# Kernel tuning notes

Hardware: AMD Instinct MI355X
Metric: run time of the kernel (lower is better)

Reference implementation:

```python
import jax, jax.numpy as jnp
import numpy as np

EMBED_DIM = 1024
NUM_HEADS = 16
HEAD_DIM = EMBED_DIM // NUM_HEADS
WINDOW = 128


def setup_inputs() -> dict:
    key = jax.random.key(0)
    ks = jax.random.split(key, 11)
    B, S, E = 2, 2048, EMBED_DIM
    scale = 1.0 / np.sqrt(E)
    inp = {
        "q": jax.random.normal(ks[0], (B, S, E), jnp.float32),
        "k": jax.random.normal(ks[1], (B, S, E), jnp.float32),
        "v": jax.random.normal(ks[2], (B, S, E), jnp.float32),
        "Wq": jax.random.normal(ks[3], (E, E), jnp.float32) * scale,
        "bq": jnp.zeros((E,), jnp.float32),
        "Wk": jax.random.normal(ks[4], (E, E), jnp.float32) * scale,
        "bk": jnp.zeros((E,), jnp.float32),
        "Wv": jax.random.normal(ks[5], (E, E), jnp.float32) * scale,
        "bv": jnp.zeros((E,), jnp.float32),
        "Wo": jax.random.normal(ks[6], (E, E), jnp.float32) * scale,
        "bo": jnp.zeros((E,), jnp.float32),
    }
    return inp


def reference(q, k, v, Wq, bq, Wk, bk, Wv, bv, Wo, bo):
    B, S, E = q.shape
    H, D = NUM_HEADS, HEAD_DIM
    # projections (torch Linear: x @ W.T + b)
    Q = (q @ Wq.T + bq).reshape(B, S, H, D).transpose(0, 2, 1, 3)  # [B,H,S,D]
    K = (k @ Wk.T + bk).reshape(B, S, H, D).transpose(0, 2, 1, 3)
    V = (v @ Wv.T + bv).reshape(B, S, H, D).transpose(0, 2, 1, 3)
    scores = jnp.einsum("bhqd,bhkd->bhqk", Q, K) / jnp.sqrt(jnp.float32(D))
    idx = jnp.arange(S)
    band = jnp.abs(idx[:, None] - idx[None, :]) <= WINDOW  # [S,S] bool band mask
    scores = jnp.where(band[None, None], scores, -jnp.inf)
    probs = jax.nn.softmax(scores, axis=-1)
    out = jnp.einsum("bhqk,bhkd->bhqd", probs, V)  # [B,H,S,D]
    out = out.transpose(0, 2, 1, 3).reshape(B, S, E)
    return out @ Wo.T + bo
```

## Files before the change

kernel.cpp:

```cpp
#include <hip/hip_runtime.h>


#define S_LEN 2048
#define EMB   1024
#define NHEAD 16
#define HDIM  64
#define MROWS 4096

typedef __attribute__((ext_vector_type(4))) float f32x4;
typedef __attribute__((ext_vector_type(8))) short bf16x8;

__device__ __forceinline__ unsigned short f2bf(float x){
  union { float f; unsigned u; } un; un.f = x;
  unsigned u = un.u;
  unsigned r = (u + 0x7FFFu + ((u >> 16) & 1u)) >> 16;
  return (unsigned short)r;
}

__global__ __launch_bounds__(256) void cvt3_kernel(
    const float4* __restrict__ s0, const float4* __restrict__ s1,
    const float4* __restrict__ s2,
    unsigned long long* __restrict__ d0, unsigned long long* __restrict__ d1,
    unsigned long long* __restrict__ d2)
{
  int i = blockIdx.x * 256 + threadIdx.x;
  const float4* s = (blockIdx.y == 0) ? s0 : (blockIdx.y == 1) ? s1 : s2;
  unsigned long long* d = (blockIdx.y == 0) ? d0 : (blockIdx.y == 1) ? d1 : d2;
  float4 v = s[i];
  d[i] = (unsigned long long)f2bf(v.x)
       | ((unsigned long long)f2bf(v.y) << 16)
       | ((unsigned long long)f2bf(v.z) << 32)
       | ((unsigned long long)f2bf(v.w) << 48);
}

__global__ __launch_bounds__(256) void cvt4_kernel(
    const float4* __restrict__ s0, const float4* __restrict__ s1,
    const float4* __restrict__ s2, const float4* __restrict__ s3,
    unsigned long long* __restrict__ d0, unsigned long long* __restrict__ d1,
    unsigned long long* __restrict__ d2, unsigned long long* __restrict__ d3)
{
  int i = blockIdx.x * 256 + threadIdx.x;
  const float4* s = (blockIdx.y == 0) ? s0 : (blockIdx.y == 1) ? s1 :
                    (blockIdx.y == 2) ? s2 : s3;
  unsigned long long* d = (blockIdx.y == 0) ? d0 : (blockIdx.y == 1) ? d1 :
                          (blockIdx.y == 2) ? d2 : d3;
  float4 v = s[i];
  d[i] = (unsigned long long)f2bf(v.x)
       | ((unsigned long long)f2bf(v.y) << 16)
       | ((unsigned long long)f2bf(v.z) << 32)
       | ((unsigned long long)f2bf(v.w) << 48);
}

__device__ __forceinline__ void async_copy16(const unsigned short* g, unsigned short* l){
  __builtin_amdgcn_global_load_lds(
      (const __attribute__((address_space(1))) unsigned int*)(const void*)g,
      (__attribute__((address_space(3))) unsigned int*)(void*)l,
      16, 0, 0);
}

__device__ __forceinline__ void gemm_core_128(
    const unsigned short* __restrict__ A,
    const unsigned short* __restrict__ Bw,
    unsigned short* lds,
    int tile_m, int tile_n, f32x4 acc[4][4])
{
  const int tid  = threadIdx.x;
  const int lane = tid & 63;
  const int wid  = tid >> 6;
  const int wm = wid >> 1, wn = wid & 1;
  const int c = lane & 15, g = lane >> 4;
  const int srow = lane >> 3, sch = lane & 7;

  unsigned short* As0 = lds;
  unsigned short* Bs0 = lds + 8192;
  unsigned short* As1 = lds + 16384;
  unsigned short* Bs1 = lds + 24576;

  auto stage = [&](unsigned short* As, unsigned short* Bs, int k0){
#pragma unroll
    for (int i = 0; i < 4; ++i){
      int row = (wid*4 + i)*8 + srow;
      int chg = sch ^ (row & 7);
      async_copy16(A  + (size_t)(tile_m + row)*EMB + k0 + chg*8, As + (wid*4 + i)*512);
      async_copy16(Bw + (size_t)(tile_n + row)*EMB + k0 + chg*8, Bs + (wid*4 + i)*512);
    }
  };

  auto compute = [&](const unsigned short* As, const unsigned short* Bs){
#pragma unroll
    for (int kk = 0; kk < 2; ++kk){
      bf16x8 af[4], bfv[4];
#pragma unroll
      for (int mi = 0; mi < 4; ++mi){
        int row = wm*64 + mi*16 + c;
        int ch  = (kk*4 + g) ^ (row & 7);
        af[mi] = *(const bf16x8*)&As[row*64 + ch*8];
      }
#pragma unroll
      for (int ni = 0; ni < 4; ++ni){
        int row = wn*64 + ni*16 + c;
        int ch  = (kk*4 + g) ^ (row & 7);
        bfv[ni] = *(const bf16x8*)&Bs[row*64 + ch*8];
      }
#pragma unroll
      for (int mi = 0; mi < 4; ++mi)
#pragma unroll
        for (int ni = 0; ni < 4; ++ni)
          acc[mi][ni] = __builtin_amdgcn_mfma_f32_16x16x32_bf16(af[mi], bfv[ni], acc[mi][ni], 0, 0, 0);
    }
  };

  stage(As0, Bs0, 0);
  __syncthreads();
  for (int t = 0; t < 16; t += 2){
    stage(As1, Bs1, (t+1)*64);
    compute(As0, Bs0);
    __syncthreads();
    if (t + 2 < 16) stage(As0, Bs0, (t+2)*64);
    compute(As1, Bs1);
    __syncthreads();
  }
}

__global__ __launch_bounds__(512, 2) void qkv_gemm_kernel(
    const unsigned short* __restrict__ qb, const unsigned short* __restrict__ kb2,
    const unsigned short* __restrict__ vb,
    const unsigned short* __restrict__ Wqb, const unsigned short* __restrict__ Wkb,
    const unsigned short* __restrict__ Wvb,
    const float* __restrict__ bq, const float* __restrict__ bk,
    const float* __restrict__ bv,
    unsigned short* __restrict__ Qp, unsigned short* __restrict__ Kp,
    unsigned short* __restrict__ Vt)
{
  __shared__ __align__(16) unsigned short lds[2][2][256*64];

  const int tid = threadIdx.x, lane = tid & 63, wid = tid >> 6;
  const int wm = wid >> 2, wn = wid & 3;
  const int c = lane & 15, g = lane >> 4;
  const int srow = lane >> 3, sch = lane & 7;

  int bid  = blockIdx.x;
  int bid2 = (bid & 7) * 24 + (bid >> 3);
  const int mx = bid2 & 15, ny = bid2 >> 4;
  const int z  = ny >> 2;
  const int tile_m = mx * 256;
  const int nloc   = (ny & 3) * 256;

  const unsigned short* A = (z == 0) ? qb  : (z == 1) ? kb2 : vb;
  const unsigned short* W = (z == 0) ? Wqb : (z == 1) ? Wkb : Wvb;
  const float*       bias = (z == 0) ? bq  : (z == 1) ? bk  : bv;

  const unsigned short* Asrc = A + (size_t)tile_m * EMB;
  const unsigned short* Bsrc = W + (size_t)nloc * EMB;

  f32x4 acc[8][4] = {};

  auto stageP = [&](int b, int k0, int p){
    int row = wid*32 + p*8 + srow;
    int ch  = sch ^ (row & 7);
    async_copy16(Asrc + (size_t)row*EMB + k0 + ch*8, &lds[b][0][(wid*32 + p*8)*64]);
    async_copy16(Bsrc + (size_t)row*EMB + k0 + ch*8, &lds[b][1][(wid*32 + p*8)*64]);
  };

  stageP(0, 0, 0); stageP(0, 0, 1); stageP(0, 0, 2); stageP(0, 0, 3);

  for (int t = 0; t < 16; ++t){
    const int cb = t & 1, nb = cb ^ 1;
    const bool pre = (t < 15);
    const int k1 = (t + 1) * 64;

    if (pre){
      stageP(nb, k1, 0);
      asm volatile("s_waitcnt vmcnt(2)" ::: "memory");
    } else {
      asm volatile("s_waitcnt vmcnt(0)" ::: "memory");
    }
    asm volatile("s_barrier" ::: "memory");

    bf16x8 bfr[4][2];
#pragma unroll
    for (int ni = 0; ni < 4; ++ni)
#pragma unroll
      for (int kk = 0; kk < 2; ++kk){
        int row = wn*64 + ni*16 + c;
        int ch  = (kk*4 + g) ^ (row & 7);
        bfr[ni][kk] = *(const bf16x8*)&lds[cb][1][row*64 + ch*8];
      }

#pragma unroll
    for (int p = 0; p < 4; ++p){
      bf16x8 af[2][2];
#pragma unroll
      for (int mi = 0; mi < 2; ++mi)
#pragma unroll
        for (int kk = 0; kk < 2; ++kk){
          int row = wm*128 + (p*2 + mi)*16 + c;
          int ch  = (kk*4 + g) ^ (row & 7);
          af[mi][kk] = *(const bf16x8*)&lds[cb][0][row*64 + ch*8];
        }
      if (pre && p < 3) stageP(nb, k1, p + 1);
      __builtin_amdgcn_s_setprio(1);
#pragma unroll
      for (int kk = 0; kk < 2; ++kk)
#pragma unroll
        for (int mi = 0; mi < 2; ++mi)
#pragma unroll
          for (int ni = 0; ni < 4; ++ni)
            acc[p*2 + mi][ni] = __builtin_amdgcn_mfma_f32_16x16x32_bf16(
                af[mi][kk], bfr[ni][kk], acc[p*2 + mi][ni], 0, 0, 0);
      __builtin_amdgcn_s_setprio(0);
    }
    asm volatile("s_barrier" ::: "memory");
  }

  if (z < 2){
    unsigned short* O = (z == 0) ? Qp : Kp;
#pragma unroll
    for (int mf = 0; mf < 8; ++mf){
      int m0 = tile_m + wm*128 + mf*16 + g*4;
      int bb = m0 >> 11, ss = m0 & 2047;
#pragma unroll
      for (int ni = 0; ni < 4; ++ni){
        int nn = nloc + wn*64 + ni*16 + c;
        int h = nn >> 6, d = nn & 63;
        float bvn = bias[nn];
        size_t base = (((size_t)bb*NHEAD + h)*S_LEN + ss)*HDIM + d;
#pragma unroll
        for (int j = 0; j < 4; ++j)
          O[base + (size_t)j*HDIM] = f2bf(acc[mf][ni][j] + bvn);
      }
    }
  } else {
#pragma unroll
    for (int mf = 0; mf < 8; ++mf){
      int m0 = tile_m + wm*128 + mf*16 + g*4;
      int bb = m0 >> 11, ss = m0 & 2047;
      int ssp = (ss & ~31) | (((ss >> 2) & 3) << 3) | (((ss >> 4) & 1) << 2);
#pragma unroll
      for (int ni = 0; ni < 4; ++ni){
        int nn = nloc + wn*64 + ni*16 + c;
        int h = nn >> 6, d = nn & 63;
        float bvn = bias[nn];
        unsigned long long pk =
              (unsigned long long)f2bf(acc[mf][ni][0] + bvn)
            | ((unsigned long long)f2bf(acc[mf][ni][1] + bvn) << 16)
            | ((unsigned long long)f2bf(acc[mf][ni][2] + bvn) << 32)
            | ((unsigned long long)f2bf(acc[mf][ni][3] + bvn) << 48);
        *(unsigned long long*)&Vt[(((size_t)bb*NHEAD + h)*HDIM + d)*S_LEN + ssp] = pk;
      }
    }
  }
}

__global__ __launch_bounds__(256) void attn_kernel(
    const unsigned short* __restrict__ Qp, const unsigned short* __restrict__ Kp,
    const unsigned short* __restrict__ Vt, unsigned short* __restrict__ X2)
{
  __shared__ __align__(16) unsigned short Kl[2][64*64];
  __shared__ __align__(16) unsigned short Vl[2][64*64];

  const int tid = threadIdx.x, lane = tid & 63, w = tid >> 6;
  const int c = lane & 15, g = lane >> 4;
  int bid0 = blockIdx.x;
  int bid = (bid0 & 7) * 128 + (bid0 >> 3);
  const int bh = bid >> 5, qt = bid & 31;
  const int qbase = qt * 64;
  const int qw = qbase + w * 16;
  const int qi = qw + c;

  const unsigned short* Kbh = Kp + (size_t)bh * S_LEN * HDIM;
  const unsigned short* Vbh = Vt + (size_t)bh * HDIM * S_LEN;

  const unsigned short* Qb = Qp + ((size_t)bh*S_LEN + qw + c)*HDIM;
  bf16x8 aq0 = *(const bf16x8*)(Qb + g*8);
  bf16x8 aq1 = *(const bf16x8*)(Qb + 32 + g*8);

  f32x4 accO[4] = {};
  float lsum = 0.f;
  const float SC = 0.18033688011112042f;

  int t0 = qbase - 128; if (t0 < 0) t0 = 0;
  int t1 = qbase + 192; if (t1 > S_LEN) t1 = S_LEN;

  const int srow = lane >> 3;
  const int sch  = (lane & 7) ^ srow;

  auto stage = [&](int buf, int kt){
#pragma unroll
    for (int i = 0; i < 2; ++i){
      int r0 = w*16 + i*8;
      async_copy16(Kbh + (size_t)(kt + r0 + srow)*HDIM + sch*8, &Kl[buf][r0*64]);
      async_copy16(Vbh + (size_t)(r0 + srow)*S_LEN + kt + sch*8, &Vl[buf][r0*64]);
    }
  };

  auto compute = [&](int buf, int kt){
    f32x4 s[4];
    __builtin_amdgcn_s_setprio(1);
#pragma unroll
    for (int f = 0; f < 4; ++f){
      const unsigned short* Kr = &Kl[buf][(f*16 + c)*64];
      bf16x8 k0 = *(const bf16x8*)(Kr + ((    g) ^ (c & 7))*8);
      bf16x8 k1 = *(const bf16x8*)(Kr + ((4 + g) ^ (c & 7))*8);
      f32x4 a = {0.f, 0.f, 0.f, 0.f};
      a = __builtin_amdgcn_mfma_f32_16x16x32_bf16(k0, aq0, a, 0, 0, 0);
      a = __builtin_amdgcn_mfma_f32_16x16x32_bf16(k1, aq1, a, 0, 0, 0);
      s[f] = a;
    }
    __builtin_amdgcn_s_setprio(0);

    float p[4][4];
    bool nomask = (kt >= qw - 113) && (kt <= qw + 65);
    if (nomask){
#pragma unroll
      for (int f = 0; f < 4; ++f)
#pragma unroll
        for (int j = 0; j < 4; ++j){
          p[f][j] = exp2f(s[f][j] * SC);
          lsum += p[f][j];
        }
    } else {
#pragma unroll
      for (int f = 0; f < 4; ++f)
#pragma unroll
        for (int j = 0; j < 4; ++j){
          int dlt = qi - (kt + f*16 + g*4 + j);
          float e = exp2f(s[f][j] * SC);
          e = (dlt <= 128 && dlt >= -128) ? e : 0.f;
          p[f][j] = e;
          lsum += e;
        }
    }

    union { unsigned u[4]; bf16x8 v; } A0, A1;
    A0.u[0] = (unsigned)f2bf(p[0][0]) | ((unsigned)f2bf(p[0][1]) << 16);
    A0.u[1] = (unsigned)f2bf(p[0][2]) | ((unsigned)f2bf(p[0][3]) << 16);
    A0.u[2] = (unsigned)f2bf(p[1][0]) | ((unsigned)f2bf(p[1][1]) << 16);
    A0.u[3] = (unsigned)f2bf(p[1][2]) | ((unsigned)f2bf(p[1][3]) << 16);
    A1.u[0] = (unsigned)f2bf(p[2][0]) | ((unsigned)f2bf(p[2][1]) << 16);
    A1.u[1] = (unsigned)f2bf(p[2][2]) | ((unsigned)f2bf(p[2][3]) << 16);
    A1.u[2] = (unsigned)f2bf(p[3][0]) | ((unsigned)f2bf(p[3][1]) << 16);
    A1.u[3] = (unsigned)f2bf(p[3][2]) | ((unsigned)f2bf(p[3][3]) << 16);

    __builtin_amdgcn_s_setprio(1);
#pragma unroll
    for (int dblk = 0; dblk < 4; ++dblk){
      const unsigned short* Vr = &Vl[buf][(dblk*16 + c)*64];
      bf16x8 v0 = *(const bf16x8*)(Vr + ((    g) ^ (c & 7))*8);
      bf16x8 v1 = *(const bf16x8*)(Vr + ((4 + g) ^ (c & 7))*8);
      accO[dblk] = __builtin_amdgcn_mfma_f32_16x16x32_bf16(A0.v, v0, accO[dblk], 0, 0, 0);
      accO[dblk] = __builtin_amdgcn_mfma_f32_16x16x32_bf16(A1.v, v1, accO[dblk], 0, 0, 0);
    }
    __builtin_amdgcn_s_setprio(0);
  };

  stage(0, t0);
  __syncthreads();
  int cur = 0;
  for (int kt = t0; kt < t1; kt += 64){
    if (kt + 64 < t1) stage(cur ^ 1, kt + 64);
    bool active = (kt + 63 >= qw - 128) && (kt <= qw + 143);
    if (active) compute(cur, kt);
    __syncthreads();
    cur ^= 1;
  }

  lsum += __shfl_xor(lsum, 16);
  lsum += __shfl_xor(lsum, 32);
  float rl[4];
#pragma unroll
  for (int j = 0; j < 4; ++j)
    rl[j] = 1.f / __shfl(lsum, g*4 + j);

  const int b_ = bh >> 4, h_ = bh & 15;
#pragma unroll
  for (int dblk = 0; dblk < 4; ++dblk)
#pragma unroll
    for (int j = 0; j < 4; ++j){
      int s_ = qw + g*4 + j, d_ = dblk*16 + c;
      X2[((size_t)(b_*S_LEN + s_))*EMB + h_*64 + d_] = f2bf(accO[dblk][j] * rl[j]);
    }
}

__global__ __launch_bounds__(256) void out_gemm_kernel(
    const unsigned short* __restrict__ X2, const unsigned short* __restrict__ Wob,
    const float* __restrict__ bo, float* __restrict__ out)
{
  __shared__ __align__(16) unsigned short lds[4*8192];
  const int tile_m = blockIdx.x * 128;
  const int tile_n = blockIdx.y * 128;
  f32x4 acc[4][4] = {};
  gemm_core_128(X2, Wob, lds, tile_m, tile_n, acc);

  const int tid = threadIdx.x, lane = tid & 63, wid = tid >> 6;
  const int wm = wid >> 1, wn = wid & 1, c = lane & 15, g = lane >> 4;
#pragma unroll
  for (int mi = 0; mi < 4; ++mi){
    int m0 = tile_m + wm*64 + mi*16 + g*4;
#pragma unroll
    for (int ni = 0; ni < 4; ++ni){
      int n = tile_n + wn*64 + ni*16 + c;
      float bvn = bo[n];
#pragma unroll
      for (int j = 0; j < 4; ++j)
        out[(size_t)(m0 + j)*EMB + n] = acc[mi][ni][j] + bvn;
    }
  }
}

extern "C" void kernel_launch(void* const* d_in, const int* in_sizes, int n_in,
                              void* d_out, int out_size, void* d_ws, size_t ws_size,
                              hipStream_t stream)
{
  const float* q  = (const float*)d_in[0];
  const float* k  = (const float*)d_in[1];
  const float* v  = (const float*)d_in[2];
  const float* Wq = (const float*)d_in[3];
  const float* bq = (const float*)d_in[4];
  const float* Wk = (const float*)d_in[5];
  const float* bk = (const float*)d_in[6];
  const float* Wv = (const float*)d_in[7];
  const float* bv = (const float*)d_in[8];
  const float* Wo = (const float*)d_in[9];
  const float* bo = (const float*)d_in[10];
  float* out = (float*)d_out;

  unsigned short* ws = (unsigned short*)d_ws;
  unsigned short* qb  = ws;
  unsigned short* kb  = ws + 4194304;
  unsigned short* vb  = ws + 8388608;
  unsigned short* Wqb = ws + 12582912;
  unsigned short* Wkb = ws + 13631488;
  unsigned short* Wvb = ws + 14680064;
  unsigned short* Wob = ws + 15728640;
  unsigned short* Qp  = ws + 16777216;
  unsigned short* Kp  = ws + 20971520;
  unsigned short* Vt  = ws + 25165824;
  unsigned short* X2  = qb;

  cvt3_kernel<<<dim3(4096, 3), 256, 0, stream>>>(
      (const float4*)q, (const float4*)k, (const float4*)v,
      (unsigned long long*)qb, (unsigned long long*)kb, (unsigned long long*)vb);
  cvt4_kernel<<<dim3(1024, 4), 256, 0, stream>>>(
      (const float4*)Wq, (const float4*)Wk, (const float4*)Wv, (const float4*)Wo,
      (unsigned long long*)Wqb, (unsigned long long*)Wkb,
      (unsigned long long*)Wvb, (unsigned long long*)Wob);

  qkv_gemm_kernel<<<dim3(192), 512, 0, stream>>>(
      qb, kb, vb, Wqb, Wkb, Wvb, bq, bk, bv, Qp, Kp, Vt);

  attn_kernel<<<1024, 256, 0, stream>>>(Qp, Kp, Vt, X2);

  out_gemm_kernel<<<dim3(32, 8), 256, 0, stream>>>(X2, Wob, bo, out);
}
```

Baseline: 86.80 us.

## Process four query tiles per attention block with a six-slot K/V ring buffer

Each attention block now handles four consecutive 64-row query tiles of one head instead of one. K/V tiles live in a six-slot LDS ring, so tiles shared by neighbouring query tiles are loaded once rather than up to five times, with prefetch of the next tile overlapping compute. The grid shrinks from 1024 to 256 blocks, which lowers parallelism and occupancy (LDS grows to 96KB per block) in exchange for less global traffic. Synchronisation uses explicit vmcnt waits and raw s_barrier.

```diff
diff --git a/kernel.cpp b/kernel.cpp
--- a/kernel.cpp
+++ b/kernel.cpp
@@ -256,130 +256,147 @@
     const unsigned short* __restrict__ Qp, const unsigned short* __restrict__ Kp,
     const unsigned short* __restrict__ Vt, unsigned short* __restrict__ X2)
 {
-  __shared__ __align__(16) unsigned short Kl[2][64*64];
-  __shared__ __align__(16) unsigned short Vl[2][64*64];
+  __shared__ __align__(16) unsigned short Kl[6][64*64];
+  __shared__ __align__(16) unsigned short Vl[6][64*64];
 
   const int tid = threadIdx.x, lane = tid & 63, w = tid >> 6;
   const int c = lane & 15, g = lane >> 4;
   int bid0 = blockIdx.x;
-  int bid = (bid0 & 7) * 128 + (bid0 >> 3);
-  const int bh = bid >> 5, qt = bid & 31;
-  const int qbase = qt * 64;
-  const int qw = qbase + w * 16;
-  const int qi = qw + c;
+  int bid = (bid0 & 7) * 32 + (bid0 >> 3);
+  const int bh = bid >> 3, qc = bid & 7;
+  const int qt0 = qc * 4;
 
   const unsigned short* Kbh = Kp + (size_t)bh * S_LEN * HDIM;
   const unsigned short* Vbh = Vt + (size_t)bh * HDIM * S_LEN;
-
-  const unsigned short* Qb = Qp + ((size_t)bh*S_LEN + qw + c)*HDIM;
-  bf16x8 aq0 = *(const bf16x8*)(Qb + g*8);
-  bf16x8 aq1 = *(const bf16x8*)(Qb + 32 + g*8);
-
-  f32x4 accO[4] = {};
-  float lsum = 0.f;
+  const int b_ = bh >> 4, h_ = bh & 15;
   const float SC = 0.18033688011112042f;
-
-  int t0 = qbase - 128; if (t0 < 0) t0 = 0;
-  int t1 = qbase + 192; if (t1 > S_LEN) t1 = S_LEN;
 
   const int srow = lane >> 3;
   const int sch  = (lane & 7) ^ srow;
 
-  auto stage = [&](int buf, int kt){
+  bf16x8 aq[4][2];
+#pragma unroll
+  for (int p = 0; p < 4; ++p){
+    const unsigned short* Qb = Qp + ((size_t)bh*S_LEN + (qt0 + p)*64 + w*16 + c)*HDIM;
+    aq[p][0] = *(const bf16x8*)(Qb + g*8);
+    aq[p][1] = *(const bf16x8*)(Qb + 32 + g*8);
+  }
+
+  auto stage = [&](int t){
+    int slot = t % 6;
+    int kt = t * 64;
 #pragma unroll
     for (int i = 0; i < 2; ++i){
       int r0 = w*16 + i*8;
-      async_copy16(Kbh + (size_t)(kt + r0 + srow)*HDIM + sch*8, &Kl[buf][r0*64]);
-      async_copy16(Vbh + (size_t)(r0 + srow)*S_LEN + kt + sch*8, &Vl[buf][r0*64]);
+      async_copy16(Kbh + (size_t)(kt + r0 + srow)*HDIM + sch*8, &Kl[slot][r0*64]);
+      async_copy16(Vbh + (size_t)(r0 + srow)*S_LEN + kt + sch*8, &Vl[slot][r0*64]);
     }
   };
 
-  auto compute = [&](int buf, int kt){
-    f32x4 s[4];
-    __builtin_amdgcn_s_setprio(1);
-#pragma unroll
-    for (int f = 0; f < 4; ++f){
-      const unsigned short* Kr = &Kl[buf][(f*16 + c)*64];
-      bf16x8 k0 = *(const bf16x8*)(Kr + ((    g) ^ (c & 7))*8);
-      bf16x8 k1 = *(const bf16x8*)(Kr + ((4 + g) ^ (c & 7))*8);
-      f32x4 a = {0.f, 0.f, 0.f, 0.f};
-      a = __builtin_amdgcn_mfma_f32_16x16x32_bf16(k0, aq0, a, 0, 0, 0);
-      a = __builtin_amdgcn_mfma_f32_16x16x32_bf16(k1, aq1, a, 0, 0, 0);
-      s[f] = a;
-    }
-    __builtin_amdgcn_s_setprio(0);
-
-    float p[4][4];
-    bool nomask = (kt >= qw - 113) && (kt <= qw + 65);
-    if (nomask){
-#pragma unroll
-      for (int f = 0; f < 4; ++f)
-#pragma unroll
-        for (int j = 0; j < 4; ++j){
-          p[f][j] = exp2f(s[f][j] * SC);
-          lsum += p[f][j];
-        }
+  {
+    int tlo = qt0 - 2; if (tlo < 0) tlo = 0;
+    for (int t = tlo; t < qt0 + 3; ++t) stage(t);
+  }
+
+#pragma unroll
+  for (int p = 0; p < 4; ++p){
+    const int qt = qt0 + p;
+    const int qp = qt * 64 + w * 16;
+    const int qi = qp + c;
+
+    if (p < 3 && qt + 3 < 32){
+      stage(qt + 3);
+      asm volatile("s_waitcnt vmcnt(4)" ::: "memory");
     } else {
-#pragma unroll
-      for (int f = 0; f < 4; ++f)
-#pragma unroll
-        for (int j = 0; j < 4; ++j){
-          int dlt = qi - (kt + f*16 + g*4 + j);
-          float e = exp2f(s[f][j] * SC);
-          e = (dlt <= 128 && dlt >= -128) ? e : 0.f;
-          p[f][j] = e;
-          lsum += e;
-        }
-    }
-
-    union { unsigned u[4]; bf16x8 v; } A0, A1;
-    A0.u[0] = (unsigned)f2bf(p[0][0]) | ((unsigned)f2bf(p[0][1]) << 16);
-    A0.u[1] = (unsigned)f2bf(p[0][2]) | ((unsigned)f2bf(p[0][3]) << 16);
-    A0.u[2] = (unsigned)f2bf(p[1][0]) | ((unsigned)f2bf(p[1][1]) << 16);
-    A0.u[3] = (unsigned)f2bf(p[1][2]) | ((unsigned)f2bf(p[1][3]) << 16);
-    A1.u[0] = (unsigned)f2bf(p[2][0]) | ((unsigned)f2bf(p[2][1]) << 16);
-    A1.u[1] = (unsigned)f2bf(p[2][2]) | ((unsigned)f2bf(p[2][3]) << 16);
-    A1.u[2] = (unsigned)f2bf(p[3][0]) | ((unsigned)f2bf(p[3][1]) << 16);
-    A1.u[3] = (unsigned)f2bf(p[3][2]) | ((unsigned)f2bf(p[3][3]) << 16);
-
-    __builtin_amdgcn_s_setprio(1);
-#pragma unroll
-    for (int dblk = 0; dblk < 4; ++dblk){
-      const unsigned short* Vr = &Vl[buf][(dblk*16 + c)*64];
-      bf16x8 v0 = *(const bf16x8*)(Vr + ((    g) ^ (c & 7))*8);
-      bf16x8 v1 = *(const bf16x8*)(Vr + ((4 + g) ^ (c & 7))*8);
-      accO[dblk] = __builtin_amdgcn_mfma_f32_16x16x32_bf16(A0.v, v0, accO[dblk], 0, 0, 0);
-      accO[dblk] = __builtin_amdgcn_mfma_f32_16x16x32_bf16(A1.v, v1, accO[dblk], 0, 0, 0);
-    }
-    __builtin_amdgcn_s_setprio(0);
-  };
-
-  stage(0, t0);
-  __syncthreads();
-  int cur = 0;
-  for (int kt = t0; kt < t1; kt += 64){
-    if (kt + 64 < t1) stage(cur ^ 1, kt + 64);
-    bool active = (kt + 63 >= qw - 128) && (kt <= qw + 143);
-    if (active) compute(cur, kt);
-    __syncthreads();
-    cur ^= 1;
-  }
-
-  lsum += __shfl_xor(lsum, 16);
-  lsum += __shfl_xor(lsum, 32);
-  float rl[4];
-#pragma unroll
-  for (int j = 0; j < 4; ++j)
-    rl[j] = 1.f / __shfl(lsum, g*4 + j);
-
-  const int b_ = bh >> 4, h_ = bh & 15;
-#pragma unroll
-  for (int dblk = 0; dblk < 4; ++dblk)
-#pragma unroll
-    for (int j = 0; j < 4; ++j){
-      int s_ = qw + g*4 + j, d_ = dblk*16 + c;
-      X2[((size_t)(b_*S_LEN + s_))*EMB + h_*64 + d_] = f2bf(accO[dblk][j] * rl[j]);
-    }
+      asm volatile("s_waitcnt vmcnt(0)" ::: "memory");
+    }
+    asm volatile("s_barrier" ::: "memory");
+
+    f32x4 accO[4] = {};
+    float lsum = 0.f;
+
+    int tlo = qt - 2; if (tlo < 0) tlo = 0;
+    int thi = qt + 3; if (thi > 32) thi = 32;
+    for (int t = tlo; t < thi; ++t){
+      int slot = t % 6;
+      int kt = t * 64;
+
+      f32x4 s[4];
+      __builtin_amdgcn_s_setprio(1);
+#pragma unroll
+      for (int f = 0; f < 4; ++f){
+        const unsigned short* Kr = &Kl[slot][(f*16 + c)*64];
+        bf16x8 k0 = *(const bf16x8*)(Kr + ((    g) ^ (c & 7))*8);
+        bf16x8 k1 = *(const bf16x8*)(Kr + ((4 + g) ^ (c & 7))*8);
+        f32x4 a = {0.f, 0.f, 0.f, 0.f};
+        a = __builtin_amdgcn_mfma_f32_16x16x32_bf16(k0, aq[p][0], a, 0, 0, 0);
+        a = __builtin_amdgcn_mfma_f32_16x16x32_bf16(k1, aq[p][1], a, 0, 0, 0);
+        s[f] = a;
+      }
+      __builtin_amdgcn_s_setprio(0);
+
+      float pr[4][4];
+      bool nomask = (kt >= qp - 113) && (kt <= qp + 65);
+      if (nomask){
+#pragma unroll
+        for (int f = 0; f < 4; ++f)
+#pragma unroll
+          for (int j = 0; j < 4; ++j){
+            pr[f][j] = exp2f(s[f][j] * SC);
+            lsum += pr[f][j];
+          }
+      } else {
+#pragma unroll
+        for (int f = 0; f < 4; ++f)
+#pragma unroll
+          for (int j = 0; j < 4; ++j){
+            int dlt = qi - (kt + f*16 + g*4 + j);
+            float e = exp2f(s[f][j] * SC);
+            e = (dlt <= 128 && dlt >= -128) ? e : 0.f;
+            pr[f][j] = e;
+            lsum += e;
+          }
+      }
+
+      union { unsigned u[4]; bf16x8 v; } A0, A1;
+      A0.u[0] = (unsigned)f2bf(pr[0][0]) | ((unsigned)f2bf(pr[0][1]) << 16);
+      A0.u[1] = (unsigned)f2bf(pr[0][2]) | ((unsigned)f2bf(pr[0][3]) << 16);
+      A0.u[2] = (unsigned)f2bf(pr[1][0]) | ((unsigned)f2bf(pr[1][1]) << 16);
+      A0.u[3] = (unsigned)f2bf(pr[1][2]) | ((unsigned)f2bf(pr[1][3]) << 16);
+      A1.u[0] = (unsigned)f2bf(pr[2][0]) | ((unsigned)f2bf(pr[2][1]) << 16);
+      A1.u[1] = (unsigned)f2bf(pr[2][2]) | ((unsigned)f2bf(pr[2][3]) << 16);
+      A1.u[2] = (unsigned)f2bf(pr[3][0]) | ((unsigned)f2bf(pr[3][1]) << 16);
+      A1.u[3] = (unsigned)f2bf(pr[3][2]) | ((unsigned)f2bf(pr[3][3]) << 16);
+
+      __builtin_amdgcn_s_setprio(1);
+#pragma unroll
+      for (int dblk = 0; dblk < 4; ++dblk){
+        const unsigned short* Vr = &Vl[slot][(dblk*16 + c)*64];
+        bf16x8 v0 = *(const bf16x8*)(Vr + ((    g) ^ (c & 7))*8);
+        bf16x8 v1 = *(const bf16x8*)(Vr + ((4 + g) ^ (c & 7))*8);
+        accO[dblk] = __builtin_amdgcn_mfma_f32_16x16x32_bf16(A0.v, v0, accO[dblk], 0, 0, 0);
+        accO[dblk] = __builtin_amdgcn_mfma_f32_16x16x32_bf16(A1.v, v1, accO[dblk], 0, 0, 0);
+      }
+      __builtin_amdgcn_s_setprio(0);
+    }
+
+    lsum += __shfl_xor(lsum, 16);
+    lsum += __shfl_xor(lsum, 32);
+    float rl[4];
+#pragma unroll
+    for (int j = 0; j < 4; ++j)
+      rl[j] = 1.f / __shfl(lsum, g*4 + j);
+
+#pragma unroll
+    for (int dblk = 0; dblk < 4; ++dblk)
+#pragma unroll
+      for (int j = 0; j < 4; ++j){
+        int s_ = qp + g*4 + j, d_ = dblk*16 + c;
+        X2[((size_t)(b_*S_LEN + s_))*EMB + h_*64 + d_] = f2bf(accO[dblk][j] * rl[j]);
+      }
+
+    asm volatile("s_barrier" ::: "memory");
+  }
 }
 
 __global__ __launch_bounds__(256) void out_gemm_kernel(
@@ -449,7 +466,7 @@
   qkv_gemm_kernel<<<dim3(192), 512, 0, stream>>>(
       qb, kb, vb, Wqb, Wkb, Wvb, bq, bk, bv, Qp, Kp, Vt);
 
-  attn_kernel<<<1024, 256, 0, stream>>>(Qp, Kp, Vt, X2);
+  attn_kernel<<<256, 256, 0, stream>>>(Qp, Kp, Vt, X2);
 
   out_gemm_kernel<<<dim3(32, 8), 256, 0, stream>>>(X2, Wob, bo, out);
 }
```

Result: slower. 92.29 us (+6.3%).
